# Optimization experiments

Hardware: AMD Instinct MI355X
Metric: run time of the kernel (lower is better)

Reference implementation:

```python
import jax, jax.numpy as jnp
import numpy as np

BRANCH, VOCAB, FFN, BATCH = 8, 256, 1024, 16384
LN_EPS = 1e-5


def setup_inputs() -> dict:
    key = jax.random.key(0)
    ks = jax.random.split(key, 7)
    x = jax.random.normal(ks[0], (BATCH, BRANCH, VOCAB), dtype=jnp.float32)
    U1 = 0.01 * jax.random.normal(ks[1], (BRANCH, VOCAB, FFN), dtype=jnp.float32)
    b1 = 0.01 * jax.random.normal(ks[2], (BRANCH, FFN), dtype=jnp.float32)
    U2 = 0.01 * jax.random.normal(ks[3], (BRANCH, FFN, VOCAB), dtype=jnp.float32)
    b2 = 0.01 * jax.random.normal(ks[4], (BRANCH, VOCAB), dtype=jnp.float32)
    ln_w = jnp.ones((VOCAB,), dtype=jnp.float32)
    ln_b = jnp.zeros((VOCAB,), dtype=jnp.float32)
    return {"x": x, "U1": U1, "b1": b1, "U2": U2, "b2": b2, "ln_w": ln_w, "ln_b": ln_b}


def _layernorm(h, w, b):
    mu = jnp.mean(h, axis=-1, keepdims=True)
    var = jnp.var(h, axis=-1, keepdims=True)
    return (h - mu) * jax.lax.rsqrt(var + LN_EPS) * w + b


def reference(x, U1, b1, U2, b2, ln_w, ln_b):
    # x: (B, N, D); branch-wise batched GEMMs via einsum (avoids explicit permutes)
    skip = x
    h = jnp.einsum('bnd,nde->bne', x, U1) + b1        # (B, N, FFN)
    h = jax.nn.gelu(h, approximate=False)
    h = jnp.einsum('bne,ned->bnd', h, U2) + b2        # (B, N, VOCAB)
    h = _layernorm(h, ln_w, ln_b)
    h = jax.nn.gelu(h, approximate=False)
    out = skip + h
    return out.reshape(BATCH, 1, BRANCH * VOCAB)
```

## Files before the change

### kernel.cpp

```cpp
#include <hip/hip_runtime.h>
#include <hip/hip_bf16.h>

#define NBR   8
#define DV    256
#define FF    1024
#define ROWS  128
#define NCHUNK 16

#define L_B1 0
#define L_B2 65536
#define L_HS 131072
#define LDS_BYTES 163840

using bf16x8 = __attribute__((ext_vector_type(8))) short;
using f32x4  = __attribute__((ext_vector_type(4))) float;

__device__ __forceinline__ unsigned short f2bf(float f) {
    unsigned int u = __builtin_bit_cast(unsigned int, f);
    unsigned int r = (u + 0x7fffu + ((u >> 16) & 1u)) >> 16;
    return (unsigned short)r;
}
__device__ __forceinline__ float bf2f(unsigned short h) {
    unsigned int u = ((unsigned int)h) << 16;
    return __builtin_bit_cast(float, u);
}
__device__ __forceinline__ float gelu_fast(float x) {
    float x2 = x * x;
    float z  = x * fmaf(x2, -0.1029434959f, -2.3022078770f);
    float e  = __builtin_amdgcn_exp2f(z);
    return x * __builtin_amdgcn_rcpf(1.0f + e);
}

#define GLL(gsrc, ldst) __builtin_amdgcn_global_load_lds((const unsigned int*)(gsrc), (unsigned int*)(ldst), 16, 0, 0)
#define MFMA16 __builtin_amdgcn_mfma_f32_16x16x32_bf16

__global__ void prep_weights(const float* __restrict__ U1, const float* __restrict__ U2,
                             unsigned short* __restrict__ w1img, unsigned short* __restrict__ w2img)
{
    const int b = blockIdx.x;
    const int n = b >> 4, cch = b & 15;
    const int tid = threadIdx.x;
    char* img1 = (char*)(w1img) + ((size_t)b << 15);
    char* img2 = (char*)(w2img) + ((size_t)b << 15);
    const float* U1n = U1 + (size_t)n * DV * FF;
    const float* U2n = U2 + (size_t)n * FF * DV;
    #pragma unroll 4
    for (int e = 0; e < 64; ++e) {
        int kk = e * 4 + (tid >> 6);
        int nn = tid & 63;
        float v = U1n[(size_t)kk * FF + cch * 64 + nn];
        unsigned off = ((unsigned)(nn * 256 + kk) * 2u) ^ (unsigned)((nn & 7) << 4);
        *(unsigned short*)(img1 + off) = f2bf(v);
    }
    #pragma unroll 4
    for (int e = 0; e < 64; ++e) {
        int nn = tid;
        float v = U2n[(size_t)(cch * 64 + e) * DV + nn];
        unsigned off = ((unsigned)(nn * 64 + e) * 2u) ^ (unsigned)((nn & 7) << 4);
        *(unsigned short*)(img2 + off) = f2bf(v);
    }
}

__global__ __launch_bounds__(512, 2)
void belayer_main(const float* __restrict__ x,
                  const unsigned short* __restrict__ w1img,
                  const unsigned short* __restrict__ w2img,
                  const float* __restrict__ b1g, const float* __restrict__ b2g,
                  const float* __restrict__ lnw, const float* __restrict__ lnb,
                  float* __restrict__ out)
{
    __shared__ __align__(16) char LDS[LDS_BYTES];
    const int tid  = threadIdx.x;
    const int lane = tid & 63;
    const int wave = tid >> 6;
    const int q = lane >> 4, c = lane & 15;
    const int n    = blockIdx.x & 7;
    const int tile = blockIdx.x >> 3;
    const int row0 = tile * ROWS;
    const int rowgrp = wave >> 1, colsel = wave & 1;
    const int rowg2  = wave >> 2, colg2  = wave & 3;
    const unsigned swz = (unsigned)((c & 7) << 4);

    const char* g1base = (const char*)w1img + ((size_t)(n * 16) << 15) + (wave << 12) + lane * 16;
    const char* g2base = (const char*)w2img + ((size_t)(n * 16) << 15) + (wave << 12) + lane * 16;

    #pragma unroll
    for (int i = 0; i < 4; ++i) GLL(g1base + (i << 10), LDS + L_B1 + (wave << 12) + (i << 10));
    #pragma unroll
    for (int i = 0; i < 4; ++i) GLL(g2base + (i << 10), LDS + L_B2 + (wave << 12) + (i << 10));

    bf16x8 A[2][8];
    #pragma unroll
    for (int rf = 0; rf < 2; ++rf) {
        const float* src = x + (((size_t)(row0 + rowgrp * 32 + rf * 16 + c)) * NBR + n) * DV + q * 8;
        #pragma unroll
        for (int ks = 0; ks < 8; ++ks) {
            f32x4 v0 = *(const f32x4*)(src + ks * 32);
            f32x4 v1 = *(const f32x4*)(src + ks * 32 + 4);
            bf16x8 h;
            h[0] = (short)f2bf(v0[0]); h[1] = (short)f2bf(v0[1]);
            h[2] = (short)f2bf(v0[2]); h[3] = (short)f2bf(v0[3]);
            h[4] = (short)f2bf(v1[0]); h[5] = (short)f2bf(v1[1]);
            h[6] = (short)f2bf(v1[2]); h[7] = (short)f2bf(v1[3]);
            A[rf][ks] = h;
        }
    }

    const unsigned nn01 = (unsigned)(colsel * 32 + c);
    const unsigned aB1e = (nn01 * 512 + q * 16) ^ swz;
    const unsigned aB1o = (nn01 * 512 + q * 16 + 64) ^ swz;
    const unsigned rr0  = (unsigned)(rowg2 * 64 + c);
    const unsigned aHe  = (rr0 * 128 + q * 16) ^ swz;
    const unsigned aHo  = (rr0 * 128 + q * 16 + 64) ^ swz;
    const unsigned nn02 = (unsigned)(colg2 * 64 + c);
    const unsigned aB2e = (nn02 * 128 + q * 16) ^ swz;
    const unsigned aB2o = (nn02 * 128 + q * 16 + 64) ^ swz;
    unsigned aW[4][2];
    #pragma unroll
    for (int r = 0; r < 4; ++r)
        #pragma unroll
        for (int cf = 0; cf < 2; ++cf)
            aW[r][cf] = (unsigned)(((rowgrp * 32 + q * 4 + r) * 128 + (colsel * 32 + cf * 16 + c) * 2)
                                   ^ ((((q & 1) * 4 + r)) << 4));

    f32x4 acc2[4][4];
    #pragma unroll
    for (int i = 0; i < 4; ++i)
        #pragma unroll
        for (int j = 0; j < 4; ++j) acc2[i][j] = (f32x4){0.f, 0.f, 0.f, 0.f};

    asm volatile("s_waitcnt vmcnt(0)" ::: "memory");
    __builtin_amdgcn_s_barrier();
    asm volatile("" ::: "memory");

#define G2_PHASE(TPREV)                                                                     \
    {                                                                                       \
        const unsigned hOff  = L_HS + ((((TPREV) & 1)) << 14);                              \
        const unsigned b2Off = L_B2 + ((((TPREV) & 1)) << 15);                              \
        _Pragma("unroll")                                                                   \
        for (int ks = 0; ks < 2; ++ks) {                                                    \
            const unsigned hb = (ks ? aHo : aHe) + hOff;                                    \
            const unsigned bb = (ks ? aB2o : aB2e) + b2Off;                                 \
            bf16x8 af[4], bfr[4];                                                           \
            _Pragma("unroll")                                                               \
            for (int rf = 0; rf < 4; ++rf) af[rf]  = *(const bf16x8*)(LDS + hb + rf * 2048);\
            _Pragma("unroll")                                                               \
            for (int cf = 0; cf < 4; ++cf) bfr[cf] = *(const bf16x8*)(LDS + bb + cf * 2048);\
            _Pragma("unroll")                                                               \
            for (int rf = 0; rf < 4; ++rf)                                                  \
                _Pragma("unroll")                                                           \
                for (int cf = 0; cf < 4; ++cf)                                              \
                    acc2[rf][cf] = MFMA16(af[rf], bfr[cf], acc2[rf][cf], 0, 0, 0);          \
        }                                                                                   \
    }

    #pragma unroll 2
    for (int t = 0; t < NCHUNK; ++t) {
        const int tsrc = (t < NCHUNK - 1) ? (t + 1) : (NCHUNK - 1);
        {
            const char* g = g1base + ((size_t)tsrc << 15);
            char* l = LDS + L_B1 + (((t + 1) & 1) << 15) + (wave << 12);
            #pragma unroll
            for (int i = 0; i < 4; ++i) GLL(g + (i << 10), l + (i << 10));
        }
        if (t >= 1) G2_PHASE(t - 1)
        asm volatile("s_waitcnt vmcnt(8)\n\ts_waitcnt lgkmcnt(0)" ::: "memory");
        __builtin_amdgcn_s_barrier();
        asm volatile("" ::: "memory");
        {
            const char* g = g2base + ((size_t)tsrc << 15);
            char* l = LDS + L_B2 + (((t + 1) & 1) << 15) + (wave << 12);
            #pragma unroll
            for (int i = 0; i < 4; ++i) GLL(g + (i << 10), l + (i << 10));
        }
        {
            const unsigned b1Off = L_B1 + ((t & 1) << 15);
            f32x4 acc1[2][2];
            #pragma unroll
            for (int i = 0; i < 2; ++i)
                #pragma unroll
                for (int j = 0; j < 2; ++j) acc1[i][j] = (f32x4){0.f, 0.f, 0.f, 0.f};
            #pragma unroll
            for (int ks = 0; ks < 8; ++ks) {
                const unsigned bb = ((ks & 1) ? aB1o : aB1e) + b1Off + (ks >> 1) * 128;
                bf16x8 b0 = *(const bf16x8*)(LDS + bb);
                bf16x8 b1 = *(const bf16x8*)(LDS + bb + 8192);
                acc1[0][0] = MFMA16(A[0][ks], b0, acc1[0][0], 0, 0, 0);
                acc1[0][1] = MFMA16(A[0][ks], b1, acc1[0][1], 0, 0, 0);
                acc1[1][0] = MFMA16(A[1][ks], b0, acc1[1][0], 0, 0, 0);
                acc1[1][1] = MFMA16(A[1][ks], b1, acc1[1][1], 0, 0, 0);
            }
            const unsigned hw = L_HS + ((t & 1) << 14);
            #pragma unroll
            for (int cf = 0; cf < 2; ++cf) {
                float b1v = b1g[n * FF + t * 64 + colsel * 32 + cf * 16 + c];
                #pragma unroll
                for (int rf = 0; rf < 2; ++rf)
                    #pragma unroll
                    for (int r = 0; r < 4; ++r) {
                        float g = gelu_fast(acc1[rf][cf][r] + b1v);
                        *(unsigned short*)(LDS + hw + aW[r][cf] + rf * 2048) = f2bf(g);
                    }
            }
        }
        asm volatile("s_waitcnt vmcnt(8)\n\ts_waitcnt lgkmcnt(0)" ::: "memory");
        __builtin_amdgcn_s_barrier();
        asm volatile("" ::: "memory");
    }
    G2_PHASE(NCHUNK - 1)

    float skp[4][4][4];
    #pragma unroll
    for (int rf = 0; rf < 4; ++rf)
        #pragma unroll
        for (int r = 0; r < 4; ++r) {
            const float* xr = x + ((size_t)(row0 + rowg2 * 64 + rf * 16 + q * 4 + r) * NBR + n) * DV;
            #pragma unroll
            for (int cf = 0; cf < 4; ++cf)
                skp[rf][cf][r] = xr[colg2 * 64 + cf * 16 + c];
        }
    float b2v[4];
    #pragma unroll
    for (int cf = 0; cf < 4; ++cf) b2v[cf] = b2g[n * DV + colg2 * 64 + cf * 16 + c];

    float sA[4][4], sQ[4][4];
    #pragma unroll
    for (int rf = 0; rf < 4; ++rf)
        #pragma unroll
        for (int r = 0; r < 4; ++r) { sA[rf][r] = 0.f; sQ[rf][r] = 0.f; }
    #pragma unroll
    for (int rf = 0; rf < 4; ++rf)
        #pragma unroll
        for (int cf = 0; cf < 4; ++cf)
            #pragma unroll
            for (int r = 0; r < 4; ++r) {
                float v = acc2[rf][cf][r] + b2v[cf];
                acc2[rf][cf][r] = v;
                sA[rf][r] += v;
                sQ[rf][r] += v * v;
            }
    #pragma unroll
    for (int m = 1; m < 16; m <<= 1)
        #pragma unroll
        for (int rf = 0; rf < 4; ++rf)
            #pragma unroll
            for (int r = 0; r < 4; ++r) {
                sA[rf][r] += __shfl_xor(sA[rf][r], m, 64);
                sQ[rf][r] += __shfl_xor(sQ[rf][r], m, 64);
            }
    float* Lred = (float*)(LDS + L_HS);
    if (c == 0) {
        #pragma unroll
        for (int rf = 0; rf < 4; ++rf)
            #pragma unroll
            for (int r = 0; r < 4; ++r) {
                int row = rowg2 * 64 + rf * 16 + q * 4 + r;
                Lred[colg2 * 128 + row]       = sA[rf][r];
                Lred[512 + colg2 * 128 + row] = sQ[rf][r];
            }
    }
    __syncthreads();
    float mu[4][4], rs[4][4];
    #pragma unroll
    for (int rf = 0; rf < 4; ++rf)
        #pragma unroll
        for (int r = 0; r < 4; ++r) {
            int row = rowg2 * 64 + rf * 16 + q * 4 + r;
            float ssum = Lred[row] + Lred[128 + row] + Lred[256 + row] + Lred[384 + row];
            float qsum = Lred[512 + row] + Lred[640 + row] + Lred[768 + row] + Lred[896 + row];
            float m_ = ssum * (1.0f / 256.0f);
            float var = qsum * (1.0f / 256.0f) - m_ * m_;
            mu[rf][r] = m_;
            rs[rf][r] = rsqrtf(var + 1e-5f);
        }
    #pragma unroll
    for (int cf = 0; cf < 4; ++cf) {
        int col = colg2 * 64 + cf * 16 + c;
        float lw = lnw[col];
        float lb = lnb[col];
        #pragma unroll
        for (int rf = 0; rf < 4; ++rf)
            #pragma unroll
            for (int r = 0; r < 4; ++r) {
                int row = rowg2 * 64 + rf * 16 + q * 4 + r;
                float v = (acc2[rf][cf][r] - mu[rf][r]) * rs[rf][r] * lw + lb;
                float g = gelu_fast(v);
                out[((size_t)(row0 + row) * NBR + n) * DV + col] = skp[rf][cf][r] + g;
            }
    }
#undef G2_PHASE
}

extern "C" void kernel_launch(void* const* d_in, const int* in_sizes, int n_in,
                              void* d_out, int out_size, void* d_ws, size_t ws_size,
                              hipStream_t stream) {
    const float* x   = (const float*)d_in[0];
    const float* U1  = (const float*)d_in[1];
    const float* b1  = (const float*)d_in[2];
    const float* U2  = (const float*)d_in[3];
    const float* b2  = (const float*)d_in[4];
    const float* lnw = (const float*)d_in[5];
    const float* lnb = (const float*)d_in[6];
    float* out = (float*)d_out;

    unsigned short* w1img = (unsigned short*)d_ws;
    unsigned short* w2img = w1img + (size_t)4 * 1024 * 1024 / 2;

    prep_weights<<<dim3(128), dim3(256), 0, stream>>>(U1, U2, w1img, w2img);
    belayer_main<<<dim3(1024), dim3(512), 0, stream>>>(x, w1img, w2img, b1, b2, lnw, lnb, out);
}
```

Measured before the change: 275.5 us.

## Warp-specialize fused MLP into separate GEMM1 and GEMM2 wave groups

```diff
diff --git a/kernel.cpp b/kernel.cpp
--- a/kernel.cpp
+++ b/kernel.cpp
@@ -19,10 +19,6 @@
     unsigned int u = __builtin_bit_cast(unsigned int, f);
     unsigned int r = (u + 0x7fffu + ((u >> 16) & 1u)) >> 16;
     return (unsigned short)r;
-}
-__device__ __forceinline__ float bf2f(unsigned short h) {
-    unsigned int u = ((unsigned int)h) << 16;
-    return __builtin_bit_cast(float, u);
 }
 __device__ __forceinline__ float gelu_fast(float x) {
     float x2 = x * x;
@@ -61,7 +57,7 @@
     }
 }
 
-__global__ __launch_bounds__(512, 2)
+__global__ __launch_bounds__(1024, 4)
 void belayer_main(const float* __restrict__ x,
                   const unsigned short* __restrict__ w1img,
                   const unsigned short* __restrict__ w2img,
@@ -73,55 +69,62 @@
     const int tid  = threadIdx.x;
     const int lane = tid & 63;
     const int wave = tid >> 6;
+    const bool isP = (wave < 8);
     const int q = lane >> 4, c = lane & 15;
     const int n    = blockIdx.x & 7;
     const int tile = blockIdx.x >> 3;
     const int row0 = tile * ROWS;
-    const int rowgrp = wave >> 1, colsel = wave & 1;
-    const int rowg2  = wave >> 2, colg2  = wave & 3;
     const unsigned swz = (unsigned)((c & 7) << 4);
 
-    const char* g1base = (const char*)w1img + ((size_t)(n * 16) << 15) + (wave << 12) + lane * 16;
-    const char* g2base = (const char*)w2img + ((size_t)(n * 16) << 15) + (wave << 12) + lane * 16;
-
+    const int sw = isP ? wave : (wave - 8);
+    const char* gbase = (isP ? (const char*)w1img : (const char*)w2img)
+                        + ((size_t)(n * NCHUNK) << 15) + (sw << 12) + lane * 16;
+    char* lbase = LDS + (isP ? L_B1 : L_B2) + (sw << 12);
+
+#define STAGE(CH, HALF) do {                                        \
+        const char* g_ = gbase + ((size_t)(CH) << 15);              \
+        char* l_ = lbase + ((unsigned)(HALF) << 15);                \
+        GLL(g_,        l_);        GLL(g_ + 1024, l_ + 1024);       \
+        GLL(g_ + 2048, l_ + 2048); GLL(g_ + 3072, l_ + 3072);       \
+    } while (0)
+
+    const int rowg = wave >> 1, colsel = wave & 1;
+    const int rowg2 = (wave - 8) >> 2, colg2 = (wave - 8) & 3;
+
+    bf16x8 A[2][8];
+    if (isP) {
+        STAGE(0, 0);
+        #pragma unroll
+        for (int rf = 0; rf < 2; ++rf) {
+            const float* src = x + (((size_t)(row0 + rowg * 32 + rf * 16 + c)) * NBR + n) * DV + q * 8;
+            #pragma unroll
+            for (int ks = 0; ks < 8; ++ks) {
+                f32x4 v0 = *(const f32x4*)(src + ks * 32);
+                f32x4 v1 = *(const f32x4*)(src + ks * 32 + 4);
+                bf16x8 h;
+                h[0] = (short)f2bf(v0[0]); h[1] = (short)f2bf(v0[1]);
+                h[2] = (short)f2bf(v0[2]); h[3] = (short)f2bf(v0[3]);
+                h[4] = (short)f2bf(v1[0]); h[5] = (short)f2bf(v1[1]);
+                h[6] = (short)f2bf(v1[2]); h[7] = (short)f2bf(v1[3]);
+                A[rf][ks] = h;
+            }
+        }
+    }
+
+    unsigned aB1[2], aW[4][2];
     #pragma unroll
-    for (int i = 0; i < 4; ++i) GLL(g1base + (i << 10), LDS + L_B1 + (wave << 12) + (i << 10));
-    #pragma unroll
-    for (int i = 0; i < 4; ++i) GLL(g2base + (i << 10), LDS + L_B2 + (wave << 12) + (i << 10));
-
-    bf16x8 A[2][8];
-    #pragma unroll
-    for (int rf = 0; rf < 2; ++rf) {
-        const float* src = x + (((size_t)(row0 + rowgrp * 32 + rf * 16 + c)) * NBR + n) * DV + q * 8;
-        #pragma unroll
-        for (int ks = 0; ks < 8; ++ks) {
-            f32x4 v0 = *(const f32x4*)(src + ks * 32);
-            f32x4 v1 = *(const f32x4*)(src + ks * 32 + 4);
-            bf16x8 h;
-            h[0] = (short)f2bf(v0[0]); h[1] = (short)f2bf(v0[1]);
-            h[2] = (short)f2bf(v0[2]); h[3] = (short)f2bf(v0[3]);
-            h[4] = (short)f2bf(v1[0]); h[5] = (short)f2bf(v1[1]);
-            h[6] = (short)f2bf(v1[2]); h[7] = (short)f2bf(v1[3]);
-            A[rf][ks] = h;
-        }
-    }
-
-    const unsigned nn01 = (unsigned)(colsel * 32 + c);
-    const unsigned aB1e = (nn01 * 512 + q * 16) ^ swz;
-    const unsigned aB1o = (nn01 * 512 + q * 16 + 64) ^ swz;
-    const unsigned rr0  = (unsigned)(rowg2 * 64 + c);
-    const unsigned aHe  = (rr0 * 128 + q * 16) ^ swz;
-    const unsigned aHo  = (rr0 * 128 + q * 16 + 64) ^ swz;
-    const unsigned nn02 = (unsigned)(colg2 * 64 + c);
-    const unsigned aB2e = (nn02 * 128 + q * 16) ^ swz;
-    const unsigned aB2o = (nn02 * 128 + q * 16 + 64) ^ swz;
-    unsigned aW[4][2];
+    for (int cf = 0; cf < 2; ++cf) {
+        unsigned nn = (unsigned)(colsel * 32 + cf * 16 + c);
+        aB1[cf] = (nn * 512 + q * 16) ^ swz;
+    }
     #pragma unroll
     for (int r = 0; r < 4; ++r)
         #pragma unroll
         for (int cf = 0; cf < 2; ++cf)
-            aW[r][cf] = (unsigned)(((rowgrp * 32 + q * 4 + r) * 128 + (colsel * 32 + cf * 16 + c) * 2)
-                                   ^ ((((q & 1) * 4 + r)) << 4));
+            aW[r][cf] = (unsigned)(((rowg * 32 + q * 4 + r) * 128 + (colsel * 32 + cf * 16 + c) * 2)
+                                   ^ (((q * 4 + r) & 7) << 4));
+    const unsigned aH  = (((unsigned)(rowg2 * 64 + c)) * 128 + q * 16) ^ swz;
+    const unsigned aB2 = (((unsigned)(colg2 * 64 + c)) * 128 + q * 16) ^ swz;
 
     f32x4 acc2[4][4];
     #pragma unroll
@@ -129,166 +132,144 @@
         #pragma unroll
         for (int j = 0; j < 4; ++j) acc2[i][j] = (f32x4){0.f, 0.f, 0.f, 0.f};
 
-    asm volatile("s_waitcnt vmcnt(0)" ::: "memory");
-    __builtin_amdgcn_s_barrier();
-    asm volatile("" ::: "memory");
-
-#define G2_PHASE(TPREV)                                                                     \
-    {                                                                                       \
-        const unsigned hOff  = L_HS + ((((TPREV) & 1)) << 14);                              \
-        const unsigned b2Off = L_B2 + ((((TPREV) & 1)) << 15);                              \
-        _Pragma("unroll")                                                                   \
-        for (int ks = 0; ks < 2; ++ks) {                                                    \
-            const unsigned hb = (ks ? aHo : aHe) + hOff;                                    \
-            const unsigned bb = (ks ? aB2o : aB2e) + b2Off;                                 \
-            bf16x8 af[4], bfr[4];                                                           \
-            _Pragma("unroll")                                                               \
-            for (int rf = 0; rf < 4; ++rf) af[rf]  = *(const bf16x8*)(LDS + hb + rf * 2048);\
-            _Pragma("unroll")                                                               \
-            for (int cf = 0; cf < 4; ++cf) bfr[cf] = *(const bf16x8*)(LDS + bb + cf * 2048);\
-            _Pragma("unroll")                                                               \
-            for (int rf = 0; rf < 4; ++rf)                                                  \
-                _Pragma("unroll")                                                           \
-                for (int cf = 0; cf < 4; ++cf)                                              \
-                    acc2[rf][cf] = MFMA16(af[rf], bfr[cf], acc2[rf][cf], 0, 0, 0);          \
-        }                                                                                   \
-    }
-
-    #pragma unroll 2
-    for (int t = 0; t < NCHUNK; ++t) {
-        const int tsrc = (t < NCHUNK - 1) ? (t + 1) : (NCHUNK - 1);
-        {
-            const char* g = g1base + ((size_t)tsrc << 15);
-            char* l = LDS + L_B1 + (((t + 1) & 1) << 15) + (wave << 12);
-            #pragma unroll
-            for (int i = 0; i < 4; ++i) GLL(g + (i << 10), l + (i << 10));
-        }
-        if (t >= 1) G2_PHASE(t - 1)
-        asm volatile("s_waitcnt vmcnt(8)\n\ts_waitcnt lgkmcnt(0)" ::: "memory");
-        __builtin_amdgcn_s_barrier();
-        asm volatile("" ::: "memory");
-        {
-            const char* g = g2base + ((size_t)tsrc << 15);
-            char* l = LDS + L_B2 + (((t + 1) & 1) << 15) + (wave << 12);
-            #pragma unroll
-            for (int i = 0; i < 4; ++i) GLL(g + (i << 10), l + (i << 10));
-        }
-        {
-            const unsigned b1Off = L_B1 + ((t & 1) << 15);
-            f32x4 acc1[2][2];
-            #pragma unroll
-            for (int i = 0; i < 2; ++i)
-                #pragma unroll
-                for (int j = 0; j < 2; ++j) acc1[i][j] = (f32x4){0.f, 0.f, 0.f, 0.f};
-            #pragma unroll
-            for (int ks = 0; ks < 8; ++ks) {
-                const unsigned bb = ((ks & 1) ? aB1o : aB1e) + b1Off + (ks >> 1) * 128;
-                bf16x8 b0 = *(const bf16x8*)(LDS + bb);
-                bf16x8 b1 = *(const bf16x8*)(LDS + bb + 8192);
-                acc1[0][0] = MFMA16(A[0][ks], b0, acc1[0][0], 0, 0, 0);
-                acc1[0][1] = MFMA16(A[0][ks], b1, acc1[0][1], 0, 0, 0);
-                acc1[1][0] = MFMA16(A[1][ks], b0, acc1[1][0], 0, 0, 0);
-                acc1[1][1] = MFMA16(A[1][ks], b1, acc1[1][1], 0, 0, 0);
-            }
-            const unsigned hw = L_HS + ((t & 1) << 14);
-            #pragma unroll
-            for (int cf = 0; cf < 2; ++cf) {
-                float b1v = b1g[n * FF + t * 64 + colsel * 32 + cf * 16 + c];
-                #pragma unroll
-                for (int rf = 0; rf < 2; ++rf)
-                    #pragma unroll
-                    for (int r = 0; r < 4; ++r) {
-                        float g = gelu_fast(acc1[rf][cf][r] + b1v);
-                        *(unsigned short*)(LDS + hw + aW[r][cf] + rf * 2048) = f2bf(g);
-                    }
-            }
-        }
-        asm volatile("s_waitcnt vmcnt(8)\n\ts_waitcnt lgkmcnt(0)" ::: "memory");
-        __builtin_amdgcn_s_barrier();
-        asm volatile("" ::: "memory");
-    }
-    G2_PHASE(NCHUNK - 1)
-
-    float skp[4][4][4];
-    #pragma unroll
-    for (int rf = 0; rf < 4; ++rf)
-        #pragma unroll
-        for (int r = 0; r < 4; ++r) {
-            const float* xr = x + ((size_t)(row0 + rowg2 * 64 + rf * 16 + q * 4 + r) * NBR + n) * DV;
+    __syncthreads();
+
+    for (int t = 0; t <= NCHUNK; ++t) {
+        if (isP) {
+            if (t < NCHUNK) {
+                if (t + 1 < NCHUNK) STAGE(t + 1, (t + 1) & 1);
+                float b1v0 = b1g[n * FF + t * 64 + colsel * 32 + c];
+                float b1v1 = b1g[n * FF + t * 64 + colsel * 32 + 16 + c];
+                const unsigned bOff = L_B1 + ((unsigned)(t & 1) << 15);
+                f32x4 acc1[2][2];
+                #pragma unroll
+                for (int i = 0; i < 2; ++i)
+                    #pragma unroll
+                    for (int j = 0; j < 2; ++j) acc1[i][j] = (f32x4){0.f, 0.f, 0.f, 0.f};
+                #pragma unroll
+                for (int ks = 0; ks < 8; ++ks) {
+                    const unsigned ka = (unsigned)((ks & 1) << 6);
+                    const unsigned ko = bOff + (unsigned)(ks >> 1) * 128;
+                    bf16x8 b0  = *(const bf16x8*)(LDS + ((aB1[0] ^ ka) + ko));
+                    bf16x8 b1f = *(const bf16x8*)(LDS + ((aB1[1] ^ ka) + ko));
+                    acc1[0][0] = MFMA16(A[0][ks], b0,  acc1[0][0], 0, 0, 0);
+                    acc1[0][1] = MFMA16(A[0][ks], b1f, acc1[0][1], 0, 0, 0);
+                    acc1[1][0] = MFMA16(A[1][ks], b0,  acc1[1][0], 0, 0, 0);
+                    acc1[1][1] = MFMA16(A[1][ks], b1f, acc1[1][1], 0, 0, 0);
+                }
+                const unsigned hw = L_HS + ((unsigned)(t & 1) << 14);
+                #pragma unroll
+                for (int cf = 0; cf < 2; ++cf) {
+                    float bv = cf ? b1v1 : b1v0;
+                    #pragma unroll
+                    for (int rf = 0; rf < 2; ++rf)
+                        #pragma unroll
+                        for (int r = 0; r < 4; ++r) {
+                            float g = gelu_fast(acc1[rf][cf][r] + bv);
+                            *(unsigned short*)(LDS + hw + aW[r][cf] + rf * 2048) = f2bf(g);
+                        }
+                }
+            }
+        } else {
+            if (t < NCHUNK) STAGE(t, t & 1);
+            if (t >= 1) {
+                const unsigned hOff  = L_HS + ((unsigned)((t - 1) & 1) << 14);
+                const unsigned b2Off = L_B2 + ((unsigned)((t - 1) & 1) << 15);
+                #pragma unroll
+                for (int ks = 0; ks < 2; ++ks) {
+                    const unsigned ka = (unsigned)(ks << 6);
+                    bf16x8 af[4], bf[4];
+                    #pragma unroll
+                    for (int rf = 0; rf < 4; ++rf)
+                        af[rf] = *(const bf16x8*)(LDS + hOff + ((aH ^ ka) + rf * 2048));
+                    #pragma unroll
+                    for (int cf = 0; cf < 4; ++cf)
+                        bf[cf] = *(const bf16x8*)(LDS + b2Off + ((aB2 ^ ka) + cf * 2048));
+                    #pragma unroll
+                    for (int rf = 0; rf < 4; ++rf)
+                        #pragma unroll
+                        for (int cf = 0; cf < 4; ++cf)
+                            acc2[rf][cf] = MFMA16(af[rf], bf[cf], acc2[rf][cf], 0, 0, 0);
+                }
+            }
+        }
+        __syncthreads();
+    }
+
+    float* Lred = (float*)(LDS + L_HS);
+    float sA[4][4], sQ[4][4];
+    if (!isP) {
+        float b2v[4];
+        #pragma unroll
+        for (int cf = 0; cf < 4; ++cf) b2v[cf] = b2g[n * DV + colg2 * 64 + cf * 16 + c];
+        #pragma unroll
+        for (int rf = 0; rf < 4; ++rf)
+            #pragma unroll
+            for (int r = 0; r < 4; ++r) { sA[rf][r] = 0.f; sQ[rf][r] = 0.f; }
+        #pragma unroll
+        for (int rf = 0; rf < 4; ++rf)
             #pragma unroll
             for (int cf = 0; cf < 4; ++cf)
-                skp[rf][cf][r] = xr[colg2 * 64 + cf * 16 + c];
-        }
-    float b2v[4];
-    #pragma unroll
-    for (int cf = 0; cf < 4; ++cf) b2v[cf] = b2g[n * DV + colg2 * 64 + cf * 16 + c];
-
-    float sA[4][4], sQ[4][4];
-    #pragma unroll
-    for (int rf = 0; rf < 4; ++rf)
-        #pragma unroll
-        for (int r = 0; r < 4; ++r) { sA[rf][r] = 0.f; sQ[rf][r] = 0.f; }
-    #pragma unroll
-    for (int rf = 0; rf < 4; ++rf)
-        #pragma unroll
-        for (int cf = 0; cf < 4; ++cf)
-            #pragma unroll
-            for (int r = 0; r < 4; ++r) {
-                float v = acc2[rf][cf][r] + b2v[cf];
-                acc2[rf][cf][r] = v;
-                sA[rf][r] += v;
-                sQ[rf][r] += v * v;
-            }
-    #pragma unroll
-    for (int m = 1; m < 16; m <<= 1)
-        #pragma unroll
-        for (int rf = 0; rf < 4; ++rf)
-            #pragma unroll
-            for (int r = 0; r < 4; ++r) {
-                sA[rf][r] += __shfl_xor(sA[rf][r], m, 64);
-                sQ[rf][r] += __shfl_xor(sQ[rf][r], m, 64);
-            }
-    float* Lred = (float*)(LDS + L_HS);
-    if (c == 0) {
+                #pragma unroll
+                for (int r = 0; r < 4; ++r) {
+                    float v = acc2[rf][cf][r] + b2v[cf];
+                    acc2[rf][cf][r] = v;
+                    sA[rf][r] += v;
+                    sQ[rf][r] += v * v;
+                }
+        #pragma unroll
+        for (int m = 1; m < 16; m <<= 1)
+            #pragma unroll
+            for (int rf = 0; rf < 4; ++rf)
+                #pragma unroll
+                for (int r = 0; r < 4; ++r) {
+                    sA[rf][r] += __shfl_xor(sA[rf][r], m, 64);
+                    sQ[rf][r] += __shfl_xor(sQ[rf][r], m, 64);
+                }
+        if (c == 0) {
+            #pragma unroll
+            for (int rf = 0; rf < 4; ++rf)
+                #pragma unroll
+                for (int r = 0; r < 4; ++r) {
+                    int row = rowg2 * 64 + rf * 16 + q * 4 + r;
+                    Lred[colg2 * 128 + row]       = sA[rf][r];
+                    Lred[512 + colg2 * 128 + row] = sQ[rf][r];
+                }
+        }
+    }
+    __syncthreads();
+    if (!isP) {
+        float mu[4][4], rs[4][4];
         #pragma unroll
         for (int rf = 0; rf < 4; ++rf)
             #pragma unroll
             for (int r = 0; r < 4; ++r) {
                 int row = rowg2 * 64 + rf * 16 + q * 4 + r;
-                Lred[colg2 * 128 + row]       = sA[rf][r];
-                Lred[512 + colg2 * 128 + row] = sQ[rf][r];
-            }
-    }
-    __syncthreads();
-    float mu[4][4], rs[4][4];
-    #pragma unroll
-    for (int rf = 0; rf < 4; ++rf)
-        #pragma unroll
-        for (int r = 0; r < 4; ++r) {
-            int row = rowg2 * 64 + rf * 16 + q * 4 + r;
-            float ssum = Lred[row] + Lred[128 + row] + Lred[256 + row] + Lred[384 + row];
-            float qsum = Lred[512 + row] + Lred[640 + row] + Lred[768 + row] + Lred[896 + row];
-            float m_ = ssum * (1.0f / 256.0f);
-            float var = qsum * (1.0f / 256.0f) - m_ * m_;
-            mu[rf][r] = m_;
-            rs[rf][r] = rsqrtf(var + 1e-5f);
-        }
-    #pragma unroll
-    for (int cf = 0; cf < 4; ++cf) {
-        int col = colg2 * 64 + cf * 16 + c;
-        float lw = lnw[col];
-        float lb = lnb[col];
-        #pragma unroll
-        for (int rf = 0; rf < 4; ++rf)
-            #pragma unroll
-            for (int r = 0; r < 4; ++r) {
-                int row = rowg2 * 64 + rf * 16 + q * 4 + r;
-                float v = (acc2[rf][cf][r] - mu[rf][r]) * rs[rf][r] * lw + lb;
-                float g = gelu_fast(v);
-                out[((size_t)(row0 + row) * NBR + n) * DV + col] = skp[rf][cf][r] + g;
-            }
-    }
-#undef G2_PHASE
+                float ssum = Lred[row] + Lred[128 + row] + Lred[256 + row] + Lred[384 + row];
+                float qsum = Lred[512 + row] + Lred[640 + row] + Lred[768 + row] + Lred[896 + row];
+                float m_ = ssum * (1.0f / 256.0f);
+                float var = qsum * (1.0f / 256.0f) - m_ * m_;
+                mu[rf][r] = m_;
+                rs[rf][r] = rsqrtf(var + 1e-5f);
+            }
+        #pragma unroll
+        for (int cf = 0; cf < 4; ++cf) {
+            int col = colg2 * 64 + cf * 16 + c;
+            float lw = lnw[col];
+            float lb = lnb[col];
+            #pragma unroll
+            for (int rf = 0; rf < 4; ++rf)
+                #pragma unroll
+                for (int r = 0; r < 4; ++r) {
+                    int row = rowg2 * 64 + rf * 16 + q * 4 + r;
+                    float v = (acc2[rf][cf][r] - mu[rf][r]) * rs[rf][r] * lw + lb;
+                    float g = gelu_fast(v);
+                    size_t oi = ((size_t)(row0 + row) * NBR + n) * DV + col;
+                    out[oi] = x[oi] + g;
+                }
+        }
+    }
+#undef STAGE
 }
 
 extern "C" void kernel_launch(void* const* d_in, const int* in_sizes, int n_in,
@@ -307,5 +288,5 @@
     unsigned short* w2img = w1img + (size_t)4 * 1024 * 1024 / 2;
 
     prep_weights<<<dim3(128), dim3(256), 0, stream>>>(U1, U2, w1img, w2img);
-    belayer_main<<<dim3(1024), dim3(512), 0, stream>>>(x, w1img, w2img, b1, b2, lnw, lnb, out);
-}
+    belayer_main<<<dim3(1024), dim3(1024), 0, stream>>>(x, w1img, w2img, b1, b2, lnw, lnb, out);
+}
```

Result: slower. 667.7 us (+142.3%).

## Restructure chunk loop into barrier-phased schedule with split LDS reads and prio

Applied to the files above, without the earlier changes.

```diff
diff --git a/kernel.cpp b/kernel.cpp
--- a/kernel.cpp
+++ b/kernel.cpp
@@ -7,10 +7,11 @@
 #define ROWS  128
 #define NCHUNK 16
 
-#define L_B1 0
-#define L_B2 65536
-#define L_HS 131072
-#define LDS_BYTES 163840
+#define L_B1   0
+#define L_B2   65536
+#define L_HS   131072
+#define L_BIAS 147456
+#define LDS_BYTES 151552
 
 using bf16x8 = __attribute__((ext_vector_type(8))) short;
 using f32x4  = __attribute__((ext_vector_type(4))) float;
@@ -19,10 +20,6 @@
     unsigned int u = __builtin_bit_cast(unsigned int, f);
     unsigned int r = (u + 0x7fffu + ((u >> 16) & 1u)) >> 16;
     return (unsigned short)r;
-}
-__device__ __forceinline__ float bf2f(unsigned short h) {
-    unsigned int u = ((unsigned int)h) << 16;
-    return __builtin_bit_cast(float, u);
 }
 __device__ __forceinline__ float gelu_fast(float x) {
     float x2 = x * x;
@@ -33,6 +30,11 @@
 
 #define GLL(gsrc, ldst) __builtin_amdgcn_global_load_lds((const unsigned int*)(gsrc), (unsigned int*)(ldst), 16, 0, 0)
 #define MFMA16 __builtin_amdgcn_mfma_f32_16x16x32_bf16
+
+#define CLOBBER() asm volatile("" ::: "memory")
+#define BAR()     do { CLOBBER(); __builtin_amdgcn_s_barrier(); CLOBBER(); } while (0)
+#define LGKM0()   do { asm volatile("s_waitcnt lgkmcnt(0)" ::: "memory"); __builtin_amdgcn_sched_barrier(0); } while (0)
+#define VMCNT(N)  asm volatile("s_waitcnt vmcnt(" #N ")" ::: "memory")
 
 __global__ void prep_weights(const float* __restrict__ U1, const float* __restrict__ U2,
                              unsigned short* __restrict__ w1img, unsigned short* __restrict__ w2img)
@@ -81,8 +83,8 @@
     const int rowg2  = wave >> 2, colg2  = wave & 3;
     const unsigned swz = (unsigned)((c & 7) << 4);
 
-    const char* g1base = (const char*)w1img + ((size_t)(n * 16) << 15) + (wave << 12) + lane * 16;
-    const char* g2base = (const char*)w2img + ((size_t)(n * 16) << 15) + (wave << 12) + lane * 16;
+    const char* g1base = (const char*)w1img + ((size_t)(n * NCHUNK) << 15) + (wave << 12) + lane * 16;
+    const char* g2base = (const char*)w2img + ((size_t)(n * NCHUNK) << 15) + (wave << 12) + lane * 16;
 
     #pragma unroll
     for (int i = 0; i < 4; ++i) GLL(g1base + (i << 10), LDS + L_B1 + (wave << 12) + (i << 10));
@@ -105,6 +107,12 @@
             A[rf][ks] = h;
         }
     }
+    {
+        float* bl = (float*)(LDS + L_BIAS);
+        bl[tid]       = b1g[n * FF + tid];
+        bl[tid + 512] = b1g[n * FF + tid + 512];
+    }
+    __syncthreads();
 
     const unsigned nn01 = (unsigned)(colsel * 32 + c);
     const unsigned aB1e = (nn01 * 512 + q * 16) ^ swz;
@@ -121,93 +129,125 @@
         #pragma unroll
         for (int cf = 0; cf < 2; ++cf)
             aW[r][cf] = (unsigned)(((rowgrp * 32 + q * 4 + r) * 128 + (colsel * 32 + cf * 16 + c) * 2)
-                                   ^ ((((q & 1) * 4 + r)) << 4));
+                                   ^ (((q * 4 + r) & 7) << 4));
 
     f32x4 acc2[4][4];
     #pragma unroll
     for (int i = 0; i < 4; ++i)
         #pragma unroll
         for (int j = 0; j < 4; ++j) acc2[i][j] = (f32x4){0.f, 0.f, 0.f, 0.f};
-
-    asm volatile("s_waitcnt vmcnt(0)" ::: "memory");
-    __builtin_amdgcn_s_barrier();
-    asm volatile("" ::: "memory");
-
-#define G2_PHASE(TPREV)                                                                     \
-    {                                                                                       \
-        const unsigned hOff  = L_HS + ((((TPREV) & 1)) << 14);                              \
-        const unsigned b2Off = L_B2 + ((((TPREV) & 1)) << 15);                              \
-        _Pragma("unroll")                                                                   \
-        for (int ks = 0; ks < 2; ++ks) {                                                    \
-            const unsigned hb = (ks ? aHo : aHe) + hOff;                                    \
-            const unsigned bb = (ks ? aB2o : aB2e) + b2Off;                                 \
-            bf16x8 af[4], bfr[4];                                                           \
-            _Pragma("unroll")                                                               \
-            for (int rf = 0; rf < 4; ++rf) af[rf]  = *(const bf16x8*)(LDS + hb + rf * 2048);\
-            _Pragma("unroll")                                                               \
-            for (int cf = 0; cf < 4; ++cf) bfr[cf] = *(const bf16x8*)(LDS + bb + cf * 2048);\
-            _Pragma("unroll")                                                               \
-            for (int rf = 0; rf < 4; ++rf)                                                  \
-                _Pragma("unroll")                                                           \
-                for (int cf = 0; cf < 4; ++cf)                                              \
-                    acc2[rf][cf] = MFMA16(af[rf], bfr[cf], acc2[rf][cf], 0, 0, 0);          \
-        }                                                                                   \
-    }
 
     #pragma unroll 2
     for (int t = 0; t < NCHUNK; ++t) {
         const int tsrc = (t < NCHUNK - 1) ? (t + 1) : (NCHUNK - 1);
+        const unsigned b1Off = L_B1 + ((unsigned)(t & 1) << 15);
+        const unsigned b2Off = L_B2 + ((unsigned)(t & 1) << 15);
+
+        VMCNT(4);
+        BAR();
+        bf16x8 p0[4], p1[4];
+        #pragma unroll
+        for (int ks = 0; ks < 4; ++ks) {
+            const unsigned bbA = ((ks & 1) ? aB1o : aB1e) + b1Off + (unsigned)(ks >> 1) * 128;
+            p0[ks] = *(const bf16x8*)(LDS + bbA);
+            p1[ks] = *(const bf16x8*)(LDS + bbA + 8192);
+        }
         {
-            const char* g = g1base + ((size_t)tsrc << 15);
-            char* l = LDS + L_B1 + (((t + 1) & 1) << 15) + (wave << 12);
-            #pragma unroll
-            for (int i = 0; i < 4; ++i) GLL(g + (i << 10), l + (i << 10));
-        }
-        if (t >= 1) G2_PHASE(t - 1)
-        asm volatile("s_waitcnt vmcnt(8)\n\ts_waitcnt lgkmcnt(0)" ::: "memory");
-        __builtin_amdgcn_s_barrier();
-        asm volatile("" ::: "memory");
-        {
-            const char* g = g2base + ((size_t)tsrc << 15);
-            char* l = LDS + L_B2 + (((t + 1) & 1) << 15) + (wave << 12);
-            #pragma unroll
-            for (int i = 0; i < 4; ++i) GLL(g + (i << 10), l + (i << 10));
-        }
-        {
-            const unsigned b1Off = L_B1 + ((t & 1) << 15);
-            f32x4 acc1[2][2];
-            #pragma unroll
-            for (int i = 0; i < 2; ++i)
+            const char* g1 = g1base + ((size_t)tsrc << 15);
+            char* l1 = LDS + L_B1 + (((t + 1) & 1) << 15) + (wave << 12);
+            #pragma unroll
+            for (int i = 0; i < 4; ++i) GLL(g1 + (i << 10), l1 + (i << 10));
+            const char* g2 = g2base + ((size_t)tsrc << 15);
+            char* l2 = LDS + L_B2 + (((t + 1) & 1) << 15) + (wave << 12);
+            #pragma unroll
+            for (int i = 0; i < 4; ++i) GLL(g2 + (i << 10), l2 + (i << 10));
+        }
+        BAR();
+
+        f32x4 acc1[2][2];
+        #pragma unroll
+        for (int i = 0; i < 2; ++i)
+            #pragma unroll
+            for (int j = 0; j < 2; ++j) acc1[i][j] = (f32x4){0.f, 0.f, 0.f, 0.f};
+        LGKM0();
+        __builtin_amdgcn_s_setprio(1);
+        #pragma unroll
+        for (int ks = 0; ks < 4; ++ks) {
+            acc1[0][0] = MFMA16(A[0][ks], p0[ks], acc1[0][0], 0, 0, 0);
+            acc1[0][1] = MFMA16(A[0][ks], p1[ks], acc1[0][1], 0, 0, 0);
+            acc1[1][0] = MFMA16(A[1][ks], p0[ks], acc1[1][0], 0, 0, 0);
+            acc1[1][1] = MFMA16(A[1][ks], p1[ks], acc1[1][1], 0, 0, 0);
+        }
+        __builtin_amdgcn_s_setprio(0);
+        bf16x8 r0[4], r1[4];
+        #pragma unroll
+        for (int ks = 4; ks < 8; ++ks) {
+            const unsigned bbA = ((ks & 1) ? aB1o : aB1e) + b1Off + (unsigned)(ks >> 1) * 128;
+            r0[ks - 4] = *(const bf16x8*)(LDS + bbA);
+            r1[ks - 4] = *(const bf16x8*)(LDS + bbA + 8192);
+        }
+        float b1v0 = *(const float*)(LDS + L_BIAS + (unsigned)(t * 64 + colsel * 32 + c) * 4);
+        float b1v1 = *(const float*)(LDS + L_BIAS + (unsigned)(t * 64 + colsel * 32 + 16 + c) * 4);
+        BAR();
+
+        LGKM0();
+        __builtin_amdgcn_s_setprio(1);
+        #pragma unroll
+        for (int ks = 0; ks < 4; ++ks) {
+            acc1[0][0] = MFMA16(A[0][ks + 4], r0[ks], acc1[0][0], 0, 0, 0);
+            acc1[0][1] = MFMA16(A[0][ks + 4], r1[ks], acc1[0][1], 0, 0, 0);
+            acc1[1][0] = MFMA16(A[1][ks + 4], r0[ks], acc1[1][0], 0, 0, 0);
+            acc1[1][1] = MFMA16(A[1][ks + 4], r1[ks], acc1[1][1], 0, 0, 0);
+        }
+        __builtin_amdgcn_s_setprio(0);
+        #pragma unroll
+        for (int cf = 0; cf < 2; ++cf) {
+            float bv = cf ? b1v1 : b1v0;
+            #pragma unroll
+            for (int rf = 0; rf < 2; ++rf)
                 #pragma unroll
-                for (int j = 0; j < 2; ++j) acc1[i][j] = (f32x4){0.f, 0.f, 0.f, 0.f};
-            #pragma unroll
-            for (int ks = 0; ks < 8; ++ks) {
-                const unsigned bb = ((ks & 1) ? aB1o : aB1e) + b1Off + (ks >> 1) * 128;
-                bf16x8 b0 = *(const bf16x8*)(LDS + bb);
-                bf16x8 b1 = *(const bf16x8*)(LDS + bb + 8192);
-                acc1[0][0] = MFMA16(A[0][ks], b0, acc1[0][0], 0, 0, 0);
-                acc1[0][1] = MFMA16(A[0][ks], b1, acc1[0][1], 0, 0, 0);
-                acc1[1][0] = MFMA16(A[1][ks], b0, acc1[1][0], 0, 0, 0);
-                acc1[1][1] = MFMA16(A[1][ks], b1, acc1[1][1], 0, 0, 0);
-            }
-            const unsigned hw = L_HS + ((t & 1) << 14);
-            #pragma unroll
-            for (int cf = 0; cf < 2; ++cf) {
-                float b1v = b1g[n * FF + t * 64 + colsel * 32 + cf * 16 + c];
-                #pragma unroll
-                for (int rf = 0; rf < 2; ++rf)
-                    #pragma unroll
-                    for (int r = 0; r < 4; ++r) {
-                        float g = gelu_fast(acc1[rf][cf][r] + b1v);
-                        *(unsigned short*)(LDS + hw + aW[r][cf] + rf * 2048) = f2bf(g);
-                    }
-            }
-        }
-        asm volatile("s_waitcnt vmcnt(8)\n\ts_waitcnt lgkmcnt(0)" ::: "memory");
-        __builtin_amdgcn_s_barrier();
-        asm volatile("" ::: "memory");
-    }
-    G2_PHASE(NCHUNK - 1)
+                for (int r = 0; r < 4; ++r) {
+                    float g = gelu_fast(acc1[rf][cf][r] + bv);
+                    *(unsigned short*)(LDS + L_HS + aW[r][cf] + rf * 2048) = f2bf(g);
+                }
+        }
+        LGKM0();
+        VMCNT(8);
+        BAR();
+
+        bf16x8 af0[4], bf0[4];
+        #pragma unroll
+        for (int rf = 0; rf < 4; ++rf) af0[rf] = *(const bf16x8*)(LDS + L_HS + aHe + rf * 2048);
+        #pragma unroll
+        for (int cf = 0; cf < 4; ++cf) bf0[cf] = *(const bf16x8*)(LDS + b2Off + aB2e + cf * 2048);
+        BAR();
+
+        LGKM0();
+        __builtin_amdgcn_s_setprio(1);
+        #pragma unroll
+        for (int rf = 0; rf < 4; ++rf)
+            #pragma unroll
+            for (int cf = 0; cf < 4; ++cf)
+                acc2[rf][cf] = MFMA16(af0[rf], bf0[cf], acc2[rf][cf], 0, 0, 0);
+        __builtin_amdgcn_s_setprio(0);
+        bf16x8 af1[4], bf1[4];
+        #pragma unroll
+        for (int rf = 0; rf < 4; ++rf) af1[rf] = *(const bf16x8*)(LDS + L_HS + aHo + rf * 2048);
+        #pragma unroll
+        for (int cf = 0; cf < 4; ++cf) bf1[cf] = *(const bf16x8*)(LDS + b2Off + aB2o + cf * 2048);
+        BAR();
+
+        LGKM0();
+        __builtin_amdgcn_s_setprio(1);
+        #pragma unroll
+        for (int rf = 0; rf < 4; ++rf)
+            #pragma unroll
+            for (int cf = 0; cf < 4; ++cf)
+                acc2[rf][cf] = MFMA16(af1[rf], bf1[cf], acc2[rf][cf], 0, 0, 0);
+        __builtin_amdgcn_s_setprio(0);
+    }
+
+    __syncthreads();
 
     float skp[4][4][4];
     #pragma unroll
@@ -288,7 +328,6 @@
                 out[((size_t)(row0 + row) * NBR + n) * DV + col] = skp[rf][cf][r] + g;
             }
     }
-#undef G2_PHASE
 }
 
 extern "C" void kernel_launch(void* const* d_in, const int* in_sizes, int n_in,
```

Measured after the change: 279.0 us. About the same (+1.2%).
